# Performance work log

Measured on AMD Instinct MI355X. Metric: run time of the kernel, lower is better.

## Reference

```python
import jax, jax.numpy as jnp
import numpy as np
from jax import lax

STRIDE = 16
ANCHOR_BASE = 16
PRE_NMS = 6000
POST_NMS = 2000
NMS_THRESH = 0.7


def _generate_anchors(base_size=16, ratios=(0.5, 1.0, 2.0), scales=(8, 16, 32)):
    w = h = float(base_size)
    x_ctr = 0.5 * (w - 1)
    y_ctr = 0.5 * (h - 1)
    size = w * h
    anchors = []
    for r in ratios:
        ws = np.round(np.sqrt(size / r))
        hs = np.round(ws * r)
        for s in scales:
            wss, hss = ws * s, hs * s
            anchors.append([x_ctr - 0.5 * (wss - 1), y_ctr - 0.5 * (hss - 1),
                            x_ctr + 0.5 * (wss - 1), y_ctr + 0.5 * (hss - 1)])
    return np.array(anchors, dtype=np.float32)  # [9,4]


def _all_anchors(width, height, stride):
    base = _generate_anchors(ANCHOR_BASE)  # [A,4]
    sx = np.arange(width, dtype=np.float32) * stride
    gy, gx = np.meshgrid(np.arange(height, dtype=np.float32) * stride, sx, indexing='ij')
    shifts = np.stack([gx.ravel(), gy.ravel(), gx.ravel(), gy.ravel()], axis=1)  # [K,4] h-major
    return jnp.asarray((shifts[:, None, :] + base[None, :, :]).reshape(-1, 4))  # [K*A,4]


def setup_inputs() -> dict:
    key = jax.random.key(0)
    k1, k2 = jax.random.split(key)
    H = W = 64
    bbox_deltas = jax.random.normal(k1, (1, 36, H, W), dtype=jnp.float32)
    scores = jax.random.uniform(k2, (1, 2, 9 * H, W), dtype=jnp.float32)
    return {"bbox_deltas": bbox_deltas, "scores": scores, "im_w": 1024, "im_h": 1024}


def reference(bbox_deltas, scores, im_w, im_h):
    H, W = bbox_deltas.shape[2], bbox_deltas.shape[3]
    # fg scores: reshape [1,2,9H,W] -> [1,18,H,W], take channels 9:18
    sc = scores.reshape(1, 18, H, W)[:, 9:, :, :].transpose(0, 2, 3, 1).reshape(-1)
    dl = bbox_deltas.transpose(0, 2, 3, 1).reshape(-1, 4)
    anchors = _all_anchors(W, H, STRIDE)

    # bbox_transform_inv (decode)
    aw = anchors[:, 2] - anchors[:, 0] + 1.0
    ah = anchors[:, 3] - anchors[:, 1] + 1.0
    acx = anchors[:, 0] + 0.5 * aw
    acy = anchors[:, 1] + 0.5 * ah
    pcx = dl[:, 0] * aw + acx
    pcy = dl[:, 1] * ah + acy
    pw = jnp.exp(dl[:, 2]) * aw
    ph = jnp.exp(dl[:, 3]) * ah
    x1 = jnp.clip(pcx - 0.5 * pw, 0.0, im_w - 1.0)
    y1 = jnp.clip(pcy - 0.5 * ph, 0.0, im_h - 1.0)
    x2 = jnp.clip(pcx + 0.5 * pw, 0.0, im_w - 1.0)
    y2 = jnp.clip(pcy + 0.5 * ph, 0.0, im_h - 1.0)
    props = jnp.stack([x1, y1, x2, y2], axis=1)

    # min-size filter
    thresh = 16.0 * (float(im_h) / float(im_w))
    keep_f = ((x2 - x1 + 1.0) >= thresh) & ((y2 - y1 + 1.0) >= thresh)
    sc_m = jnp.where(keep_f, sc, -jnp.inf)

    # pre-NMS top-k by score
    top_sc, idx = lax.top_k(sc_m, PRE_NMS)
    top_p = props[idx]  # [PRE_NMS,4], sorted by score desc
    valid = jnp.isfinite(top_sc)

    # pairwise IoU (with +1 box convention, as in py_cpu_nms)
    bx1, by1, bx2, by2 = top_p[:, 0], top_p[:, 1], top_p[:, 2], top_p[:, 3]
    areas = (bx2 - bx1 + 1.0) * (by2 - by1 + 1.0)
    iw = jnp.maximum(jnp.minimum(bx2[:, None], bx2[None, :]) - jnp.maximum(bx1[:, None], bx1[None, :]) + 1.0, 0.0)
    ih = jnp.maximum(jnp.minimum(by2[:, None], by2[None, :]) - jnp.maximum(by1[:, None], by1[None, :]) + 1.0, 0.0)
    inter = iw * ih
    iou = inter / (areas[:, None] + areas[None, :] - inter)
    sup = iou > NMS_THRESH  # [N,N]

    ar = jnp.arange(PRE_NMS)

    def body(i, keep):
        row = sup[i] & keep[i] & (ar > i)
        return keep & (~row)

    keep = lax.fori_loop(0, PRE_NMS, body, valid)

    # take first POST_NMS kept (in score order), scatter into fixed-size output
    rank = jnp.cumsum(keep.astype(jnp.int32)) - 1
    sel = keep & (rank < POST_NMS)
    dst = jnp.where(sel, rank, POST_NMS)  # invalid rows dumped into slot POST_NMS
    out_b = jnp.zeros((POST_NMS + 1, 4), dtype=jnp.float32).at[dst].set(
        jnp.where(sel[:, None], top_p, 0.0))[:POST_NMS]
    out_s = jnp.zeros((POST_NMS + 1,), dtype=jnp.float32).at[dst].set(
        jnp.where(sel, top_sc, 0.0))[:POST_NMS]
    blob = jnp.concatenate([jnp.zeros((POST_NMS, 1), dtype=jnp.float32), out_b], axis=1)
    return blob, out_s[:, None]
```

## Files before the change

### kernel.cpp

```cpp
#include <hip/hip_runtime.h>
#include <math.h>

typedef unsigned int u32;
typedef unsigned long long u64;

#define NANCH   36864
#define PRE     6000
#define POST    2000
#define NWORDS  94
#define NSTEP   47
#define ROWSP   6016

#define OFF_PROPS   ((size_t)0)
#define OFF_SV      ((size_t)589824)
#define OFF_SORTED  ((size_t)884736)
#define OFF_SEL     ((size_t)932864)
#define OFF_MASKT   ((size_t)1227776)
#define OFF_CTRL    ((size_t)5751808)
#define OFF_H1      ((size_t)5752064)

__device__ __constant__ float BA[9][4] = {
  {-84.f,-40.f,99.f,55.f},   {-176.f,-88.f,191.f,103.f}, {-360.f,-184.f,375.f,199.f},
  {-56.f,-56.f,71.f,71.f},   {-120.f,-120.f,135.f,135.f},{-248.f,-248.f,263.f,263.f},
  {-36.f,-80.f,51.f,95.f},   {-80.f,-168.f,95.f,183.f},  {-168.f,-344.f,183.f,359.f}};

__device__ __forceinline__ u32 key_bin(u32 key) {
  if (key < 0xBF000000u) return 0u;
  u32 b = ((key >> 13) - 0x5F800u) + 1u;
  return b > 1024u ? 1024u : b;
}

__global__ void decode_k(const float* __restrict__ deltas, const float* __restrict__ scores,
                         const int* __restrict__ imw_p, const int* __restrict__ imh_p,
                         float4* __restrict__ props, u64* __restrict__ sortvals,
                         u32* __restrict__ h1, u32* __restrict__ ctrl) {
  #pragma clang fp contract(off)
  if (threadIdx.x == 0) ctrl[6] = 0u;
  int i = blockIdx.x * 256 + threadIdx.x;
  if (i >= NANCH) return;
  int a = i % 9;
  int pix = i / 9;
  int x = pix & 63, y = pix >> 6;

  float sc = scores[(9 + a) * 4096 + pix];
  float d0 = deltas[(a * 4 + 0) * 4096 + pix];
  float d1 = deltas[(a * 4 + 1) * 4096 + pix];
  float d2 = deltas[(a * 4 + 2) * 4096 + pix];
  float d3 = deltas[(a * 4 + 3) * 4096 + pix];

  float gx = (float)(x * 16), gy = (float)(y * 16);
  float ax1 = gx + BA[a][0], ay1 = gy + BA[a][1];
  float ax2 = gx + BA[a][2], ay2 = gy + BA[a][3];
  float aw = ax2 - ax1 + 1.0f, ah = ay2 - ay1 + 1.0f;
  float acx = ax1 + 0.5f * aw, acy = ay1 + 0.5f * ah;

  float pcx = d0 * aw + acx;
  float pcy = d1 * ah + acy;
  float pw = (float)exp((double)d2) * aw;
  float ph = (float)exp((double)d3) * ah;

  float imw1 = (float)imw_p[0] - 1.0f, imh1 = (float)imh_p[0] - 1.0f;
  float x1 = fminf(fmaxf(pcx - 0.5f * pw, 0.0f), imw1);
  float y1 = fminf(fmaxf(pcy - 0.5f * ph, 0.0f), imh1);
  float x2 = fminf(fmaxf(pcx + 0.5f * pw, 0.0f), imw1);
  float y2 = fminf(fmaxf(pcy + 0.5f * ph, 0.0f), imh1);
  props[i] = make_float4(x1, y1, x2, y2);

  float thresh = 16.0f * ((float)imh_p[0] / (float)imw_p[0]);
  bool keep = (x2 - x1 + 1.0f >= thresh) && (y2 - y1 + 1.0f >= thresh);
  u32 key = keep ? (__float_as_uint(sc) | 0x80000000u) : 0u;
  sortvals[i] = ((u64)key << 32) | (u64)(0xFFFFFFFFu - (u32)i);
  u32 bin = key_bin(key);
  if (bin) atomicAdd(&h1[bin], 1u);
}

__global__ void compact_k(const u64* __restrict__ sv, const u32* __restrict__ h1,
                          u32* __restrict__ ctrl, u64* __restrict__ sel) {
  __shared__ u32 Lchosen;
  int t = threadIdx.x;
  if (t < 64) {
    int l = t;
    u32 loc[16], suf[16];
    #pragma unroll
    for (int k = 0; k < 16; ++k) loc[k] = h1[1 + l * 16 + k];
    u32 acc = 0;
    #pragma unroll
    for (int k = 15; k >= 0; --k) { acc += loc[k]; suf[k] = acc; }
    u32 sfx = acc;
    for (int off = 1; off < 64; off <<= 1) {
      u32 o = __shfl_down(sfx, off);
      if (l + off < 64) sfx += o;
    }
    u32 S_above = sfx - acc;
    u64 mball = __ballot(suf[0] + S_above >= (u32)PRE);
    if (mball == 0ULL) { if (l == 0) Lchosen = 0u; }
    else {
      int L = 63 - __builtin_clzll(mball);
      if (l == L) {
        int kk = 0;
        for (int k = 15; k >= 0; --k)
          if (suf[k] + S_above >= (u32)PRE) { kk = k; break; }
        Lchosen = (u32)(1 + 16 * L + kk);
      }
    }
  }
  __syncthreads();
  u32 chosen = Lchosen;
  int i = blockIdx.x * 256 + t;
  if (i >= NANCH) return;
  u64 v = sv[i];
  if (key_bin((u32)(v >> 32)) >= chosen) {
    u32 p = atomicAdd(&ctrl[6], 1u);
    sel[p] = v;
  }
}

__global__ void rank_k(const u64* __restrict__ sel, const u32* __restrict__ ctrl,
                       u64* __restrict__ sorted) {
  __shared__ u64 sj[256];
  u32 n = ctrl[6];
  int i = blockIdx.x * 256 + threadIdx.x;
  if ((u32)(blockIdx.x * 256) >= n) return;
  u64 vi = ((u32)i < n) ? sel[i] : 0ULL;
  u32 cnt = 0;
  for (u32 jb = 0; jb < n; jb += 256) {
    __syncthreads();
    if (jb + threadIdx.x < n) sj[threadIdx.x] = sel[jb + threadIdx.x];
    __syncthreads();
    u32 m = min(256u, n - jb);
    #pragma unroll 8
    for (u32 j = 0; j < m; ++j) cnt += (u32)(sj[j] > vi);
  }
  if ((u32)i < n && cnt < (u32)PRE) sorted[cnt] = vi;
}

__global__ void mask_k(const u64* __restrict__ sorted, const float4* __restrict__ props,
                       u64* __restrict__ maskT) {
  #pragma clang fp contract(off)
  __shared__ float4 cb[64];
  int jb = blockIdx.x;
  if (jb < (int)blockIdx.y) return;
  int i = blockIdx.y * 64 + threadIdx.x;
  int jj = jb * 64 + threadIdx.x;
  float4 cc = make_float4(0.f, 0.f, 0.f, 0.f);
  if (jj < PRE) {
    u64 v = sorted[jj];
    cc = props[0xFFFFu - ((u32)v & 0xFFFFu)];
  }
  cb[threadIdx.x] = cc;
  __syncthreads();
  if (i >= PRE) return;
  u64 vi = sorted[i];
  float4 b = props[0xFFFFu - ((u32)vi & 0xFFFFu)];
  float ai = (b.z - b.x + 1.0f) * (b.w - b.y + 1.0f);
  u64 bits = 0ULL;
  int jmax = min(64, PRE - jb * 64);
  for (int j = 0; j < jmax; ++j) {
    float4 c = cb[j];
    float aj = (c.z - c.x + 1.0f) * (c.w - c.y + 1.0f);
    float iw = fmaxf(fminf(b.z, c.z) - fmaxf(b.x, c.x) + 1.0f, 0.0f);
    float ih = fmaxf(fminf(b.w, c.w) - fmaxf(b.y, c.y) + 1.0f, 0.0f);
    float inter = iw * ih;
    float iou = inter / (ai + aj - inter);
    bits |= ((u64)(iou > 0.7f)) << j;
  }
  maskT[(size_t)jb * ROWSP + i] = bits;
}

__device__ __forceinline__ u64 rl64(u64 v, int lane) {
  u32 lo = (u32)__builtin_amdgcn_readlane((int)(u32)v, lane);
  u32 hi = (u32)__builtin_amdgcn_readlane((int)(u32)(v >> 32), lane);
  return ((u64)hi << 32) | (u64)lo;
}

__global__ void __launch_bounds__(1024) nms_scan_k(const u64* __restrict__ maskT,
                                                   const u64* __restrict__ sorted,
                                                   const float4* __restrict__ props,
                                                   float* __restrict__ out) {
  __shared__ u64 Lrem[NWORDS];
  __shared__ u64 Ldiag[128][2];
  __shared__ u64 Lkb[NWORDS];
  __shared__ u64 LkA, LkB;
  __shared__ int Lstop;
  __shared__ u32 Lpre[NWORDS];
  const int t = threadIdx.x;
  const int g = t >> 7;
  const int w = t & 127;
  const bool loader = (w < NWORDS);
  u64 rv = 0;
  u64 B0[16], B1[16];
  int kept = 0;

#define ISSUE(bb, BUF) \
  if ((bb) < NSTEP && loader) { \
    const u64* p_ = maskT + (size_t)w * ROWSP + (bb) * 128 + g * 16; \
    _Pragma("unroll") \
    for (int k = 0; k < 16; ++k) BUF[k] = p_[k]; \
  }

  ISSUE(0, B0)
  ISSUE(1, B1)

  if (t < NWORDS) { Lrem[t] = 0ULL; Lkb[t] = 0ULL; }
  if (t == 0) Lstop = 0;
  __syncthreads();
  for (int r = t; r < PRE; r += 1024)
    if ((u32)(sorted[r] >> 32) == 0u)
      atomicOr((unsigned long long*)&Lrem[r >> 6], 1ULL << (r & 63));
  if (t == 0)
    atomicOr((unsigned long long*)&Lrem[NWORDS - 1],
             ~((1ULL << (PRE - (NWORDS - 1) * 64)) - 1ULL));
  __syncthreads();

#define STEP(bb, BUF) { \
    const int A_ = 2 * (bb), Bw_ = A_ + 1; \
    if (w == A_ || w == Bw_) {            \
      atomicOr((u32*)&Lrem[w], (u32)rv); \
      atomicOr(((u32*)&Lrem[w]) + 1, (u32)(rv >> 32)); \
      const int c_ = (w == Bw_); \
      _Pragma("unroll") \
      for (int k = 0; k < 16; ++k) { \
        int i_ = g * 16 + k; \
        if (c_ || i_ < 64) Ldiag[i_][c_] = BUF[k]; \
      } \
    } \
    __syncthreads();                      \
    if (t < 64) { \
      u64 a0 = Ldiag[t][0], b0 = Ldiag[t][1], b1 = Ldiag[64 + t][1]; \
      u64 availA = ~Lrem[A_]; \
      u64 availB = ~Lrem[Bw_]; \
      u64 kbA = 0, kbB = 0; \
      while (availA) { \
        int i_ = __builtin_ctzll(availA); \
        kbA |= 1ULL << i_; \
        availA &= ~rl64(a0, i_) & ~((2ULL << i_) - 1ULL);  \
        availB &= ~rl64(b0, i_); \
      } \
      while (availB) { \
        int i_ = __builtin_ctzll(availB); \
        kbB |= 1ULL << i_; \
        availB &= ~rl64(b1, i_) & ~((2ULL << i_) - 1ULL); \
      } \
      if (t == 0) { \
        Lkb[A_] = kbA; Lkb[Bw_] = kbB; LkA = kbA; LkB = kbB; \
        kept += (int)__popcll(kbA) + (int)__popcll(kbB); \
        if (kept >= POST) Lstop = 1; \
      } \
    } \
    __syncthreads();                      \
    { \
      u64 kA_ = LkA, kB_ = LkB; \
      _Pragma("unroll") \
      for (int k = 0; k < 16; ++k) { \
        int i_ = g * 16 + k; \
        u64 bit_ = (i_ < 64) ? (kA_ >> i_) : (kB_ >> (i_ - 64)); \
        rv |= (0ULL - (bit_ & 1ULL)) & BUF[k]; \
      } \
    } \
    ISSUE((bb) + 2, BUF)                  \
    if (Lstop) break; }

  for (int bb = 0; bb < NSTEP; bb += 2) {
    STEP(bb, B0)
    if (bb + 1 < NSTEP) STEP(bb + 1, B1)
  }
#undef ISSUE
#undef STEP

  __syncthreads();
  for (int i = t; i < 12000; i += 1024) out[i] = 0.0f;
  if (t == 0) {
    u32 run = 0;
    for (int w2 = 0; w2 < NWORDS; ++w2) { Lpre[w2] = run; run += (u32)__popcll(Lkb[w2]); }
  }
  __syncthreads();
  for (int i = t; i < PRE; i += 1024) {
    u64 word = Lkb[i >> 6];
    if ((word >> (i & 63)) & 1ULL) {
      u32 rank = Lpre[i >> 6] + (u32)__popcll(word & ((1ULL << (i & 63)) - 1ULL));
      if (rank < POST) {
        u64 v = sorted[i];
        float4 b = props[0xFFFFu - ((u32)v & 0xFFFFu)];
        out[rank * 5 + 1] = b.x;
        out[rank * 5 + 2] = b.y;
        out[rank * 5 + 3] = b.z;
        out[rank * 5 + 4] = b.w;
        out[10000 + rank] = __uint_as_float((u32)(v >> 32) & 0x7FFFFFFFu);
      }
    }
  }
}

extern "C" void kernel_launch(void* const* d_in, const int* in_sizes, int n_in,
                              void* d_out, int out_size, void* d_ws, size_t ws_size,
                              hipStream_t stream) {
  const float* deltas = (const float*)d_in[0];
  const float* scores = (const float*)d_in[1];
  const int* imw = (const int*)d_in[2];
  const int* imh = (const int*)d_in[3];
  char* ws = (char*)d_ws;

  float4* props   = (float4*)(ws + OFF_PROPS);
  u64*    svals   = (u64*)(ws + OFF_SV);
  u64*    sorted  = (u64*)(ws + OFF_SORTED);
  u64*    sel     = (u64*)(ws + OFF_SEL);
  u64*    maskT   = (u64*)(ws + OFF_MASKT);
  u32*    ctrl    = (u32*)(ws + OFF_CTRL);
  u32*    h1      = (u32*)(ws + OFF_H1);

  hipMemsetAsync(h1, 0, 1025 * sizeof(u32), stream);

  decode_k<<<144, 256, 0, stream>>>(deltas, scores, imw, imh, props, svals, h1, ctrl);
  compact_k<<<144, 256, 0, stream>>>(svals, h1, ctrl, sel);
  rank_k<<<144, 256, 0, stream>>>(sel, ctrl, sorted);

  dim3 mgrid(NWORDS, NWORDS);
  mask_k<<<mgrid, 64, 0, stream>>>(sorted, props, maskT);

  nms_scan_k<<<1, 1024, 0, stream>>>(maskT, sorted, props, (float*)d_out);
}
```

Before: 378.8 us.

## Fuse all proposal stages into one cooperative kernel with grid syncs

Replaces the memset plus five kernel launches with a single cooperative kernel of 94 blocks that uses grid.sync between decode, histogram compaction, rank sort, IoU mask build and the serial NMS scan. The rank sort is split across blocks by row and column chunks and accumulated with atomics, and the mask build uses wave shuffles instead of shared memory. The scan now processes one 64-bit word per step with a three-deep prefetch instead of two words per step. This removes launch gaps but adds grid-wide barrier costs, and the scan does more serial steps.

```diff
diff --git a/kernel.cpp b/kernel.cpp
--- a/kernel.cpp
+++ b/kernel.cpp
@@ -1,5 +1,8 @@
 #include <hip/hip_runtime.h>
+#include <hip/hip_cooperative_groups.h>
 #include <math.h>
+
+namespace cg = cooperative_groups;
 
 typedef unsigned int u32;
 typedef unsigned long long u64;
@@ -8,8 +11,10 @@
 #define PRE     6000
 #define POST    2000
 #define NWORDS  94
-#define NSTEP   47
 #define ROWSP   6016
+#define NBLK    94
+#define NTHR    1024
+#define GSZ     (NBLK * NTHR)
 
 #define OFF_PROPS   ((size_t)0)
 #define OFF_SV      ((size_t)589824)
@@ -30,54 +35,86 @@
   return b > 1024u ? 1024u : b;
 }
 
-__global__ void decode_k(const float* __restrict__ deltas, const float* __restrict__ scores,
-                         const int* __restrict__ imw_p, const int* __restrict__ imh_p,
-                         float4* __restrict__ props, u64* __restrict__ sortvals,
-                         u32* __restrict__ h1, u32* __restrict__ ctrl) {
+__device__ __forceinline__ u64 rl64(u64 v, int lane) {
+  u32 lo = (u32)__builtin_amdgcn_readlane((int)(u32)v, lane);
+  u32 hi = (u32)__builtin_amdgcn_readlane((int)(u32)(v >> 32), lane);
+  return ((u64)hi << 32) | (u64)lo;
+}
+
+__global__ void __launch_bounds__(1024) fused_k(const float* __restrict__ deltas,
+                                                const float* __restrict__ scores,
+                                                const int* __restrict__ imw_p,
+                                                const int* __restrict__ imh_p,
+                                                char* __restrict__ ws,
+                                                float* __restrict__ out) {
   #pragma clang fp contract(off)
-  if (threadIdx.x == 0) ctrl[6] = 0u;
-  int i = blockIdx.x * 256 + threadIdx.x;
-  if (i >= NANCH) return;
-  int a = i % 9;
-  int pix = i / 9;
-  int x = pix & 63, y = pix >> 6;
-
-  float sc = scores[(9 + a) * 4096 + pix];
-  float d0 = deltas[(a * 4 + 0) * 4096 + pix];
-  float d1 = deltas[(a * 4 + 1) * 4096 + pix];
-  float d2 = deltas[(a * 4 + 2) * 4096 + pix];
-  float d3 = deltas[(a * 4 + 3) * 4096 + pix];
-
-  float gx = (float)(x * 16), gy = (float)(y * 16);
-  float ax1 = gx + BA[a][0], ay1 = gy + BA[a][1];
-  float ax2 = gx + BA[a][2], ay2 = gy + BA[a][3];
-  float aw = ax2 - ax1 + 1.0f, ah = ay2 - ay1 + 1.0f;
-  float acx = ax1 + 0.5f * aw, acy = ay1 + 0.5f * ah;
-
-  float pcx = d0 * aw + acx;
-  float pcy = d1 * ah + acy;
-  float pw = (float)exp((double)d2) * aw;
-  float ph = (float)exp((double)d3) * ah;
-
-  float imw1 = (float)imw_p[0] - 1.0f, imh1 = (float)imh_p[0] - 1.0f;
-  float x1 = fminf(fmaxf(pcx - 0.5f * pw, 0.0f), imw1);
-  float y1 = fminf(fmaxf(pcy - 0.5f * ph, 0.0f), imh1);
-  float x2 = fminf(fmaxf(pcx + 0.5f * pw, 0.0f), imw1);
-  float y2 = fminf(fmaxf(pcy + 0.5f * ph, 0.0f), imh1);
-  props[i] = make_float4(x1, y1, x2, y2);
-
-  float thresh = 16.0f * ((float)imh_p[0] / (float)imw_p[0]);
-  bool keep = (x2 - x1 + 1.0f >= thresh) && (y2 - y1 + 1.0f >= thresh);
-  u32 key = keep ? (__float_as_uint(sc) | 0x80000000u) : 0u;
-  sortvals[i] = ((u64)key << 32) | (u64)(0xFFFFFFFFu - (u32)i);
-  u32 bin = key_bin(key);
-  if (bin) atomicAdd(&h1[bin], 1u);
-}
-
-__global__ void compact_k(const u64* __restrict__ sv, const u32* __restrict__ h1,
-                          u32* __restrict__ ctrl, u64* __restrict__ sel) {
+  float4* props  = (float4*)(ws + OFF_PROPS);
+  u64*    svals  = (u64*)(ws + OFF_SV);
+  u64*    sorted = (u64*)(ws + OFF_SORTED);
+  u64*    sel    = (u64*)(ws + OFF_SEL);
+  u64*    maskT  = (u64*)(ws + OFF_MASKT);
+  u32*    rank0  = (u32*)(ws + OFF_MASKT);
+  u32*    ctrl   = (u32*)(ws + OFF_CTRL);
+  u32*    h1     = (u32*)(ws + OFF_H1);
+
+  cg::grid_group grid = cg::this_grid();
+  const int t = threadIdx.x;
+  const int b = blockIdx.x;
+  const int gid = b * NTHR + t;
+
+  __shared__ u64 SJ[1024];
   __shared__ u32 Lchosen;
-  int t = threadIdx.x;
+  __shared__ u64 Lrem[NWORDS];
+  __shared__ u64 Ldiag[64];
+  __shared__ u64 Lkb[NWORDS];
+  __shared__ u64 LkA;
+  __shared__ int Lstop;
+  __shared__ u32 Lpre[NWORDS];
+
+  if (gid < 1025) h1[gid] = 0u;
+  if (gid < 64) ctrl[gid] = 0u;
+  if (gid < NANCH) rank0[gid] = 0u;
+  grid.sync();
+
+  if (gid < NANCH) {
+    int i = gid;
+    int a = i % 9;
+    int pix = i / 9;
+    int x = pix & 63, y = pix >> 6;
+
+    float sc = scores[(9 + a) * 4096 + pix];
+    float d0 = deltas[(a * 4 + 0) * 4096 + pix];
+    float d1 = deltas[(a * 4 + 1) * 4096 + pix];
+    float d2 = deltas[(a * 4 + 2) * 4096 + pix];
+    float d3 = deltas[(a * 4 + 3) * 4096 + pix];
+
+    float gx = (float)(x * 16), gy = (float)(y * 16);
+    float ax1 = gx + BA[a][0], ay1 = gy + BA[a][1];
+    float ax2 = gx + BA[a][2], ay2 = gy + BA[a][3];
+    float aw = ax2 - ax1 + 1.0f, ah = ay2 - ay1 + 1.0f;
+    float acx = ax1 + 0.5f * aw, acy = ay1 + 0.5f * ah;
+
+    float pcx = d0 * aw + acx;
+    float pcy = d1 * ah + acy;
+    float pw = (float)exp((double)d2) * aw;
+    float ph = (float)exp((double)d3) * ah;
+
+    float imw1 = (float)imw_p[0] - 1.0f, imh1 = (float)imh_p[0] - 1.0f;
+    float x1 = fminf(fmaxf(pcx - 0.5f * pw, 0.0f), imw1);
+    float y1 = fminf(fmaxf(pcy - 0.5f * ph, 0.0f), imh1);
+    float x2 = fminf(fmaxf(pcx + 0.5f * pw, 0.0f), imw1);
+    float y2 = fminf(fmaxf(pcy + 0.5f * ph, 0.0f), imh1);
+    props[i] = make_float4(x1, y1, x2, y2);
+
+    float thresh = 16.0f * ((float)imh_p[0] / (float)imw_p[0]);
+    bool keep = (x2 - x1 + 1.0f >= thresh) && (y2 - y1 + 1.0f >= thresh);
+    u32 key = keep ? (__float_as_uint(sc) | 0x80000000u) : 0u;
+    svals[i] = ((u64)key << 32) | (u64)(0xFFFFFFFFu - (u32)i);
+    u32 bin = key_bin(key);
+    if (bin) atomicAdd(&h1[bin], 1u);
+  }
+  grid.sync();
+
   if (t < 64) {
     int l = t;
     u32 loc[16], suf[16];
@@ -105,187 +142,175 @@
     }
   }
   __syncthreads();
-  u32 chosen = Lchosen;
-  int i = blockIdx.x * 256 + t;
-  if (i >= NANCH) return;
-  u64 v = sv[i];
-  if (key_bin((u32)(v >> 32)) >= chosen) {
-    u32 p = atomicAdd(&ctrl[6], 1u);
-    sel[p] = v;
-  }
-}
-
-__global__ void rank_k(const u64* __restrict__ sel, const u32* __restrict__ ctrl,
-                       u64* __restrict__ sorted) {
-  __shared__ u64 sj[256];
+  if (gid < 12000) out[gid] = 0.0f;
+  {
+    u32 chosen = Lchosen;
+    if (gid < NANCH) {
+      u64 v = svals[gid];
+      if (key_bin((u32)(v >> 32)) >= chosen) {
+        u32 p = atomicAdd(&ctrl[6], 1u);
+        sel[p] = v;
+      }
+    }
+  }
+  grid.sync();
+
   u32 n = ctrl[6];
-  int i = blockIdx.x * 256 + threadIdx.x;
-  if ((u32)(blockIdx.x * 256) >= n) return;
-  u64 vi = ((u32)i < n) ? sel[i] : 0ULL;
-  u32 cnt = 0;
-  for (u32 jb = 0; jb < n; jb += 256) {
+  if (b < 90) {
+    const int ic = b / 15, jc = b % 15;
+    const u32 chunk = (n + 14u) / 15u;
+    const u32 j0 = jc * chunk, j1 = min(j0 + chunk, n);
+    const u32 base_i = (u32)(ic * 1024 + t);
+    u64 vi[6]; u32 cnt[6]; int ni = 0;
+    for (u32 ii = base_i; ii < n && ni < 6; ii += 6144u) { vi[ni] = sel[ii]; cnt[ni] = 0; ++ni; }
+    for (u32 jb = j0; jb < j1; jb += 1024u) {
+      __syncthreads();
+      if (jb + (u32)t < j1) SJ[t] = sel[jb + t];
+      __syncthreads();
+      u32 m = min(1024u, j1 - jb);
+      for (u32 j = 0; j < m; ++j) {
+        u64 s = SJ[j];
+        for (int q = 0; q < ni; ++q) cnt[q] += (u32)(s > vi[q]);
+      }
+    }
+    for (int q = 0; q < ni; ++q)
+      if (cnt[q]) atomicAdd(&rank0[base_i + (u32)q * 6144u], cnt[q]);
+  }
+  grid.sync();
+
+  for (u32 ii = (u32)gid; ii < n; ii += (u32)GSZ) {
+    u32 r = rank0[ii];
+    if (r < (u32)PRE) sorted[r] = sel[ii];
+  }
+  grid.sync();
+
+  {
+    const int ib = b;
+    const int sub = t >> 6, lane = t & 63;
+    const int i = ib * 64 + lane;
+    float4 bb = make_float4(0.f, 0.f, 0.f, 0.f);
+    float ai = 1.0f;
+    const bool rowok = (i < PRE);
+    if (rowok) {
+      u64 v = sorted[i];
+      bb = props[0xFFFFu - ((u32)v & 0xFFFFu)];
+      ai = (bb.z - bb.x + 1.0f) * (bb.w - bb.y + 1.0f);
+    }
+    for (int jb = ib + sub; jb < NWORDS; jb += 16) {
+      int jj = jb * 64 + lane;
+      float4 cl = make_float4(0.f, 0.f, 0.f, 0.f);
+      if (jj < PRE) {
+        u64 v = sorted[jj];
+        cl = props[0xFFFFu - ((u32)v & 0xFFFFu)];
+      }
+      u64 bits = 0ULL;
+      for (int j = 0; j < 64; ++j) {
+        float cx1 = __shfl(cl.x, j), cy1 = __shfl(cl.y, j);
+        float cx2 = __shfl(cl.z, j), cy2 = __shfl(cl.w, j);
+        float aj = (cx2 - cx1 + 1.0f) * (cy2 - cy1 + 1.0f);
+        float iw = fmaxf(fminf(bb.z, cx2) - fmaxf(bb.x, cx1) + 1.0f, 0.0f);
+        float ih = fmaxf(fminf(bb.w, cy2) - fmaxf(bb.y, cy1) + 1.0f, 0.0f);
+        float inter = iw * ih;
+        float iou = inter / (ai + aj - inter);
+        bits |= ((u64)(iou > 0.7f)) << j;
+      }
+      if (rowok) maskT[(size_t)jb * ROWSP + i] = bits;
+    }
+  }
+  grid.sync();
+
+  if (b != 0) return;
+
+  {
+    const int g = t & 7;
+    const int w = t >> 3;
+    const bool loader = (w < NWORDS);
+    u64 rv = 0;
+    u64 A0[8], A1[8], A2[8];
+    int kept = 0;
+    if (t < NWORDS) { Lrem[t] = 0ULL; Lkb[t] = 0ULL; }
+    if (t == 0) Lstop = 0;
     __syncthreads();
-    if (jb + threadIdx.x < n) sj[threadIdx.x] = sel[jb + threadIdx.x];
+    for (int r = t; r < PRE; r += NTHR)
+      if ((u32)(sorted[r] >> 32) == 0u)
+        atomicOr((unsigned long long*)&Lrem[r >> 6], 1ULL << (r & 63));
+    if (t == 0)
+      atomicOr((unsigned long long*)&Lrem[NWORDS - 1],
+               ~((1ULL << (PRE - (NWORDS - 1) * 64)) - 1ULL));
     __syncthreads();
-    u32 m = min(256u, n - jb);
-    #pragma unroll 8
-    for (u32 j = 0; j < m; ++j) cnt += (u32)(sj[j] > vi);
-  }
-  if ((u32)i < n && cnt < (u32)PRE) sorted[cnt] = vi;
-}
-
-__global__ void mask_k(const u64* __restrict__ sorted, const float4* __restrict__ props,
-                       u64* __restrict__ maskT) {
-  #pragma clang fp contract(off)
-  __shared__ float4 cb[64];
-  int jb = blockIdx.x;
-  if (jb < (int)blockIdx.y) return;
-  int i = blockIdx.y * 64 + threadIdx.x;
-  int jj = jb * 64 + threadIdx.x;
-  float4 cc = make_float4(0.f, 0.f, 0.f, 0.f);
-  if (jj < PRE) {
-    u64 v = sorted[jj];
-    cc = props[0xFFFFu - ((u32)v & 0xFFFFu)];
-  }
-  cb[threadIdx.x] = cc;
-  __syncthreads();
-  if (i >= PRE) return;
-  u64 vi = sorted[i];
-  float4 b = props[0xFFFFu - ((u32)vi & 0xFFFFu)];
-  float ai = (b.z - b.x + 1.0f) * (b.w - b.y + 1.0f);
-  u64 bits = 0ULL;
-  int jmax = min(64, PRE - jb * 64);
-  for (int j = 0; j < jmax; ++j) {
-    float4 c = cb[j];
-    float aj = (c.z - c.x + 1.0f) * (c.w - c.y + 1.0f);
-    float iw = fmaxf(fminf(b.z, c.z) - fmaxf(b.x, c.x) + 1.0f, 0.0f);
-    float ih = fmaxf(fminf(b.w, c.w) - fmaxf(b.y, c.y) + 1.0f, 0.0f);
-    float inter = iw * ih;
-    float iou = inter / (ai + aj - inter);
-    bits |= ((u64)(iou > 0.7f)) << j;
-  }
-  maskT[(size_t)jb * ROWSP + i] = bits;
-}
-
-__device__ __forceinline__ u64 rl64(u64 v, int lane) {
-  u32 lo = (u32)__builtin_amdgcn_readlane((int)(u32)v, lane);
-  u32 hi = (u32)__builtin_amdgcn_readlane((int)(u32)(v >> 32), lane);
-  return ((u64)hi << 32) | (u64)lo;
-}
-
-__global__ void __launch_bounds__(1024) nms_scan_k(const u64* __restrict__ maskT,
-                                                   const u64* __restrict__ sorted,
-                                                   const float4* __restrict__ props,
-                                                   float* __restrict__ out) {
-  __shared__ u64 Lrem[NWORDS];
-  __shared__ u64 Ldiag[128][2];
-  __shared__ u64 Lkb[NWORDS];
-  __shared__ u64 LkA, LkB;
-  __shared__ int Lstop;
-  __shared__ u32 Lpre[NWORDS];
-  const int t = threadIdx.x;
-  const int g = t >> 7;
-  const int w = t & 127;
-  const bool loader = (w < NWORDS);
-  u64 rv = 0;
-  u64 B0[16], B1[16];
-  int kept = 0;
 
 #define ISSUE(bb, BUF) \
-  if ((bb) < NSTEP && loader) { \
-    const u64* p_ = maskT + (size_t)w * ROWSP + (bb) * 128 + g * 16; \
-    _Pragma("unroll") \
-    for (int k = 0; k < 16; ++k) BUF[k] = p_[k]; \
-  }
-
-  ISSUE(0, B0)
-  ISSUE(1, B1)
-
-  if (t < NWORDS) { Lrem[t] = 0ULL; Lkb[t] = 0ULL; }
-  if (t == 0) Lstop = 0;
-  __syncthreads();
-  for (int r = t; r < PRE; r += 1024)
-    if ((u32)(sorted[r] >> 32) == 0u)
-      atomicOr((unsigned long long*)&Lrem[r >> 6], 1ULL << (r & 63));
-  if (t == 0)
-    atomicOr((unsigned long long*)&Lrem[NWORDS - 1],
-             ~((1ULL << (PRE - (NWORDS - 1) * 64)) - 1ULL));
-  __syncthreads();
+    if ((bb) < NWORDS && loader && w >= (bb)) { \
+      const u64* p_ = maskT + (size_t)w * ROWSP + (bb) * 64 + g * 8; \
+      _Pragma("unroll") \
+      for (int k = 0; k < 8; ++k) BUF[k] = p_[k]; \
+    }
 
 #define STEP(bb, BUF) { \
-    const int A_ = 2 * (bb), Bw_ = A_ + 1; \
-    if (w == A_ || w == Bw_) {            \
-      atomicOr((u32*)&Lrem[w], (u32)rv); \
-      atomicOr(((u32*)&Lrem[w]) + 1, (u32)(rv >> 32)); \
-      const int c_ = (w == Bw_); \
+    if (w == (bb)) {                      \
+      atomicOr((u32*)&Lrem[(bb)], (u32)rv); \
+      atomicOr(((u32*)&Lrem[(bb)]) + 1, (u32)(rv >> 32)); \
       _Pragma("unroll") \
-      for (int k = 0; k < 16; ++k) { \
-        int i_ = g * 16 + k; \
-        if (c_ || i_ < 64) Ldiag[i_][c_] = BUF[k]; \
-      } \
+      for (int k = 0; k < 8; ++k) Ldiag[g * 8 + k] = BUF[k]; \
     } \
     __syncthreads();                      \
     if (t < 64) { \
-      u64 a0 = Ldiag[t][0], b0 = Ldiag[t][1], b1 = Ldiag[64 + t][1]; \
-      u64 availA = ~Lrem[A_]; \
-      u64 availB = ~Lrem[Bw_]; \
-      u64 kbA = 0, kbB = 0; \
-      while (availA) { \
-        int i_ = __builtin_ctzll(availA); \
-        kbA |= 1ULL << i_; \
-        availA &= ~rl64(a0, i_) & ~((2ULL << i_) - 1ULL);  \
-        availB &= ~rl64(b0, i_); \
-      } \
-      while (availB) { \
-        int i_ = __builtin_ctzll(availB); \
-        kbB |= 1ULL << i_; \
-        availB &= ~rl64(b1, i_) & ~((2ULL << i_) - 1ULL); \
+      u64 dgl = Ldiag[t]; \
+      u64 avail = ~Lrem[(bb)]; \
+      u64 kb = 0; \
+      while (avail) { \
+        int i_ = __builtin_ctzll(avail); \
+        kb |= 1ULL << i_; \
+        avail &= ~rl64(dgl, i_) & ~((2ULL << i_) - 1ULL);  \
       } \
       if (t == 0) { \
-        Lkb[A_] = kbA; Lkb[Bw_] = kbB; LkA = kbA; LkB = kbB; \
-        kept += (int)__popcll(kbA) + (int)__popcll(kbB); \
+        Lkb[(bb)] = kb; LkA = kb; \
+        kept += (int)__popcll(kb); \
         if (kept >= POST) Lstop = 1; \
       } \
     } \
     __syncthreads();                      \
-    { \
-      u64 kA_ = LkA, kB_ = LkB; \
+    if (loader && w > (bb)) { \
+      u64 kb_ = LkA; \
       _Pragma("unroll") \
-      for (int k = 0; k < 16; ++k) { \
-        int i_ = g * 16 + k; \
-        u64 bit_ = (i_ < 64) ? (kA_ >> i_) : (kB_ >> (i_ - 64)); \
-        rv |= (0ULL - (bit_ & 1ULL)) & BUF[k]; \
+      for (int k = 0; k < 8; ++k) { \
+        u64 bit_ = (kb_ >> (g * 8 + k)) & 1ULL; \
+        rv |= (0ULL - bit_) & BUF[k]; \
       } \
     } \
-    ISSUE((bb) + 2, BUF)                  \
+    ISSUE((bb) + 3, BUF) \
     if (Lstop) break; }
 
-  for (int bb = 0; bb < NSTEP; bb += 2) {
-    STEP(bb, B0)
-    if (bb + 1 < NSTEP) STEP(bb + 1, B1)
-  }
+    ISSUE(0, A0)
+    ISSUE(1, A1)
+    ISSUE(2, A2)
+    for (int bb = 0; bb < NWORDS; bb += 3) {
+      STEP(bb, A0)
+      if (bb + 1 < NWORDS) STEP(bb + 1, A1)
+      if (bb + 2 < NWORDS) STEP(bb + 2, A2)
+    }
 #undef ISSUE
 #undef STEP
 
-  __syncthreads();
-  for (int i = t; i < 12000; i += 1024) out[i] = 0.0f;
-  if (t == 0) {
-    u32 run = 0;
-    for (int w2 = 0; w2 < NWORDS; ++w2) { Lpre[w2] = run; run += (u32)__popcll(Lkb[w2]); }
-  }
-  __syncthreads();
-  for (int i = t; i < PRE; i += 1024) {
-    u64 word = Lkb[i >> 6];
-    if ((word >> (i & 63)) & 1ULL) {
-      u32 rank = Lpre[i >> 6] + (u32)__popcll(word & ((1ULL << (i & 63)) - 1ULL));
-      if (rank < POST) {
-        u64 v = sorted[i];
-        float4 b = props[0xFFFFu - ((u32)v & 0xFFFFu)];
-        out[rank * 5 + 1] = b.x;
-        out[rank * 5 + 2] = b.y;
-        out[rank * 5 + 3] = b.z;
-        out[rank * 5 + 4] = b.w;
-        out[10000 + rank] = __uint_as_float((u32)(v >> 32) & 0x7FFFFFFFu);
+    __syncthreads();
+    if (t == 0) {
+      u32 run = 0;
+      for (int w2 = 0; w2 < NWORDS; ++w2) { Lpre[w2] = run; run += (u32)__popcll(Lkb[w2]); }
+    }
+    __syncthreads();
+    for (int i = t; i < PRE; i += NTHR) {
+      u64 word = Lkb[i >> 6];
+      if ((word >> (i & 63)) & 1ULL) {
+        u32 rank = Lpre[i >> 6] + (u32)__popcll(word & ((1ULL << (i & 63)) - 1ULL));
+        if (rank < POST) {
+          u64 v = sorted[i];
+          float4 bx = props[0xFFFFu - ((u32)v & 0xFFFFu)];
+          out[rank * 5 + 1] = bx.x;
+          out[rank * 5 + 2] = bx.y;
+          out[rank * 5 + 3] = bx.z;
+          out[rank * 5 + 4] = bx.w;
+          out[10000 + rank] = __uint_as_float((u32)(v >> 32) & 0x7FFFFFFFu);
+        }
       }
     }
   }
@@ -299,23 +324,10 @@
   const int* imw = (const int*)d_in[2];
   const int* imh = (const int*)d_in[3];
   char* ws = (char*)d_ws;
-
-  float4* props   = (float4*)(ws + OFF_PROPS);
-  u64*    svals   = (u64*)(ws + OFF_SV);
-  u64*    sorted  = (u64*)(ws + OFF_SORTED);
-  u64*    sel     = (u64*)(ws + OFF_SEL);
-  u64*    maskT   = (u64*)(ws + OFF_MASKT);
-  u32*    ctrl    = (u32*)(ws + OFF_CTRL);
-  u32*    h1      = (u32*)(ws + OFF_H1);
-
-  hipMemsetAsync(h1, 0, 1025 * sizeof(u32), stream);
-
-  decode_k<<<144, 256, 0, stream>>>(deltas, scores, imw, imh, props, svals, h1, ctrl);
-  compact_k<<<144, 256, 0, stream>>>(svals, h1, ctrl, sel);
-  rank_k<<<144, 256, 0, stream>>>(sel, ctrl, sorted);
-
-  dim3 mgrid(NWORDS, NWORDS);
-  mask_k<<<mgrid, 64, 0, stream>>>(sorted, props, maskT);
-
-  nms_scan_k<<<1, 1024, 0, stream>>>(maskT, sorted, props, (float*)d_out);
+  float* out = (float*)d_out;
+
+  void* args[] = { (void*)&deltas, (void*)&scores, (void*)&imw, (void*)&imh,
+                   (void*)&ws, (void*)&out };
+  hipLaunchCooperativeKernel((const void*)fused_k, dim3(NBLK), dim3(NTHR),
+                             args, 0, stream);
 }
```

After: 435.0 us. +14.8%, slower.
